# Performance work log

Measured on AMD Instinct MI355X. Metric: run time of the kernel, lower is better.

## Reference

```python
import jax, jax.numpy as jnp
import numpy as np

DIM = 1280
HEADS = 16
HD = DIM // HEADS  # 80
NSEG = 8
LSEG = 1024
SEQ = NSEG * LSEG  # 8192


def _rotate_half(x):
    x1, x2 = jnp.split(x, 2, axis=-1)
    return jnp.concatenate([-x2, x1], axis=-1)


def setup_inputs() -> dict:
    key = jax.random.key(0)
    ks = jax.random.split(key, 6)
    hidden_states = jax.random.normal(ks[0], (SEQ, DIM), dtype=jnp.float32)
    # rotary embedding table: per-position angles over head_dim
    inv_freq = 1.0 / (10000.0 ** (np.arange(0, HD, 2, dtype=np.float32) / HD))
    pos = np.arange(SEQ, dtype=np.float32)
    freqs = np.outer(pos, inv_freq)                    # [SEQ, HD/2]
    emb = np.concatenate([freqs, freqs], axis=-1)      # [SEQ, HD]
    cos = jnp.asarray(np.cos(emb), dtype=jnp.float32)
    sin = jnp.asarray(np.sin(emb), dtype=jnp.float32)
    w_scale = 1.0 / np.sqrt(DIM)
    qkv_w = jax.random.normal(ks[1], (DIM, 3 * DIM), dtype=jnp.float32) * w_scale
    qkv_b = jax.random.normal(ks[2], (3 * DIM,), dtype=jnp.float32) * 0.02
    proj_w = jax.random.normal(ks[3], (DIM, DIM), dtype=jnp.float32) * w_scale
    proj_b = jax.random.normal(ks[4], (DIM,), dtype=jnp.float32) * 0.02
    cu_seqlens = jnp.arange(NSEG + 1, dtype=jnp.int32) * LSEG
    return {
        "hidden_states": hidden_states,
        "cos": cos,
        "sin": sin,
        "qkv_w": qkv_w,
        "qkv_b": qkv_b,
        "proj_w": proj_w,
        "proj_b": proj_b,
        "cu_seqlens": cu_seqlens,
    }


def reference(hidden_states, cos, sin, qkv_w, qkv_b, proj_w, proj_b, cu_seqlens):
    S, D = hidden_states.shape
    n_seg = cu_seqlens.shape[0] - 1          # static
    L = S // n_seg                            # equal-length packed segments
    # fused QKV projection: [S, 3D] -> q, k, v each [S, H, hd]
    qkv = hidden_states @ qkv_w + qkv_b
    q, k, v = (t.reshape(S, HEADS, HD) for t in jnp.split(qkv, 3, axis=-1))
    # RoPE (computed in fp32, as in apply_rotary_pos_emb_vision)
    c = cos.astype(jnp.float32)[:, None, :]   # [S, 1, hd]
    s = sin.astype(jnp.float32)[:, None, :]
    qf = q.astype(jnp.float32)
    kf = k.astype(jnp.float32)
    q = (qf * c + _rotate_half(qf) * s).astype(q.dtype)
    k = (kf * c + _rotate_half(kf) * s).astype(k.dtype)
    # block-diagonal varlen attention == independent attention per segment
    qs = q.reshape(n_seg, L, HEADS, HD)
    ks = k.reshape(n_seg, L, HEADS, HD)
    vs = v.reshape(n_seg, L, HEADS, HD)
    scale = HD ** -0.5
    scores = jnp.einsum("nqhd,nkhd->nhqk", qs, ks) * scale
    probs = jax.nn.softmax(scores.astype(jnp.float32), axis=-1).astype(qs.dtype)
    out = jnp.einsum("nhqk,nkhd->nqhd", probs, vs)     # [n, L, H, hd]
    out = out.reshape(S, D)
    return out @ proj_w + proj_b
```

## Files before the change

### kernel.cpp

```cpp
#include <hip/hip_runtime.h>

#define SEQ   8192
#define DIM   1280
#define HEADS 16
#define HD    80
#define LSEG  1024
#define QKVD  3840

typedef unsigned short USHORT;
typedef __attribute__((ext_vector_type(8))) short bf16x8;
typedef __attribute__((ext_vector_type(4))) float f32x4;
typedef __attribute__((ext_vector_type(4))) USHORT u16x4;
typedef __attribute__((ext_vector_type(4))) int i32x4;

#define CSF  0.16129832f

__device__ __forceinline__ USHORT f2bf(float x) {
  unsigned u = __float_as_uint(x);
  u += 0x7fffu + ((u >> 16) & 1u);
  return (USHORT)(u >> 16);
}
__device__ __forceinline__ float bf2f(USHORT b) {
  return __uint_as_float(((unsigned)b) << 16);
}
__device__ __forceinline__ void gload16(const void* g, void* l) {
  __builtin_amdgcn_global_load_lds(
      (const __attribute__((address_space(1))) void*)g,
      (__attribute__((address_space(3))) void*)l, 16, 0, 0);
}
__device__ __forceinline__ unsigned cvtpk(float a, float b) {
  unsigned d;
  asm("v_cvt_pk_bf16_f32 %0, %1, %2" : "=v"(d) : "v"(a), "v"(b));
  return d;
}
#define SB() __builtin_amdgcn_sched_barrier(0)

__global__ __launch_bounds__(256) void prep1(
    const float* __restrict__ hs, USHORT* __restrict__ hsB,
    const float* __restrict__ qkv_w, USHORT* __restrict__ qkvwT,
    const float* __restrict__ proj_w, USHORT* __restrict__ pwT) {
  __shared__ float tb[32][33];
  const int bx = blockIdx.x;
  const int tid = threadIdx.x;
  if (bx < 10240) {
    const int i = bx * 256 + tid;
    const float4 v = reinterpret_cast<const float4*>(hs)[i];
    USHORT* o = hsB + (size_t)i * 4;
    o[0] = f2bf(v.x); o[1] = f2bf(v.y); o[2] = f2bf(v.z); o[3] = f2bf(v.w);
    return;
  }
  const float* W; USHORT* T; int K, N, n0, k0;
  if (bx < 15040) {
    const int b = bx - 10240;
    W = qkv_w; T = qkvwT; K = DIM; N = QKVD;
    n0 = (b % 120) * 32; k0 = (b / 120) * 32;
  } else {
    const int b = bx - 15040;
    W = proj_w; T = pwT; K = DIM; N = DIM;
    n0 = (b % 40) * 32; k0 = (b / 40) * 32;
  }
  const int c = tid & 31, r0 = tid >> 5;
  for (int r = r0; r < 32; r += 8) tb[r][c] = W[(size_t)(k0 + r) * N + n0 + c];
  __syncthreads();
  for (int r = r0; r < 32; r += 8)
    T[(size_t)(n0 + r) * K + k0 + c] = f2bf(tb[c][r]);
}

__global__ __launch_bounds__(256) void prep2(
    USHORT* __restrict__ qkv, const float* __restrict__ cosb,
    const float* __restrict__ sinb, uint4* __restrict__ zb) {
  const int bx = blockIdx.x;
  const int tid = threadIdx.x;
  if (bx < 10240) {
    int idx = bx * 256 + tid;
    const int d4 = (idx % 10) * 4;
    int t = idx / 10;
    const int h = t % HEADS;
    t /= HEADS;
    const int qk = t & 1;
    const int s = t >> 1;
    USHORT* base = qkv + (size_t)s * QKVD + qk * DIM + h * HD;
    const u16x4 x1 = *(const u16x4*)&base[d4];
    const u16x4 x2 = *(const u16x4*)&base[d4 + 40];
    const f32x4 c1 = *(const f32x4*)&cosb[s * HD + d4];
    const f32x4 s1 = *(const f32x4*)&sinb[s * HD + d4];
    const f32x4 c2 = *(const f32x4*)&cosb[s * HD + d4 + 40];
    const f32x4 s2 = *(const f32x4*)&sinb[s * HD + d4 + 40];
    u16x4 o1, o2;
#pragma unroll
    for (int j = 0; j < 4; ++j) {
      const float a = bf2f(x1[j]), b = bf2f(x2[j]);
      o1[j] = f2bf(a * c1[j] - b * s1[j]);
      o2[j] = f2bf(b * c2[j] + a * s2[j]);
    }
    *(u16x4*)&base[d4] = o1;
    *(u16x4*)&base[d4 + 40] = o2;
    return;
  }
  if (tid < 64) zb[tid] = uint4{0u, 0u, 0u, 0u};
}

__global__ __launch_bounds__(512, 1) void mfma_gemm256(
    const USHORT* __restrict__ Ah, const USHORT* __restrict__ Bh,
    const float* __restrict__ bias, USHORT* __restrict__ Cout,
    USHORT* __restrict__ VtGo, int M, int N, int K, int lda) {
  extern __shared__ USHORT sm[];

  const int tid = threadIdx.x;
  const int l = tid & 63;
  const int w = tid >> 6;
  const int fr = l & 15;
  const int g = l >> 4;
  const int nrow = M >> 8;
  const int nwg = nrow * (N >> 7);
  const int orig = blockIdx.x;
  const int wg = (orig & 7) * (nwg >> 3) + (orig >> 3);
  const int row0 = (wg % nrow) << 8;
  const int col0 = (wg / nrow) << 7;
  const int wr = (w >> 1) << 6;
  const int wc = (w & 1) << 6;

  const f32x4 fz = {0.f, 0.f, 0.f, 0.f};
  f32x4 acc[4][4];
#pragma unroll
  for (int m = 0; m < 4; ++m)
#pragma unroll
    for (int n = 0; n < 4; ++n) acc[m][n] = fz;

  const int NT = K >> 6;

  const USHORT* asrc[4];
  const USHORT* bsrc[2];
#pragma unroll
  for (int i = 0; i < 4; ++i) {
    const int u = i * 512 + tid;
    const int row = u >> 3;
    const int c = (u & 7) ^ (row & 7);
    asrc[i] = Ah + (size_t)(row0 + row) * lda + c * 8;
  }
#pragma unroll
  for (int i = 0; i < 2; ++i) {
    const int u = i * 512 + tid;
    const int row = u >> 3;
    const int c = (u & 7) ^ (row & 7);
    bsrc[i] = Bh + (size_t)(col0 + row) * K + c * 8;
  }
  auto stage = [&](int b) {
#pragma unroll
    for (int i = 0; i < 4; ++i)
      gload16(asrc[i], sm + b * 16384 + (i * 512 + (w << 6)) * 8);
#pragma unroll
    for (int i = 0; i < 2; ++i)
      gload16(bsrc[i], sm + 49152 + b * 8192 + (i * 512 + (w << 6)) * 8);
  };
  auto advance = [&]() {
#pragma unroll
    for (int i = 0; i < 4; ++i) asrc[i] += 64;
#pragma unroll
    for (int i = 0; i < 2; ++i) bsrc[i] += 64;
  };

  const int fb = fr & 7;
  int aOff[2], bOff[2];
#pragma unroll
  for (int ks = 0; ks < 2; ++ks) {
    const int sl = (((ks << 2) + g) ^ fb) << 3;
    aOff[ks] = (wr + fr) * 64 + sl;
    bOff[ks] = 49152 + (wc + fr) * 64 + sl;
  }

  stage(0); advance();
  stage(1); advance();

  int cur = 0, sb = 2;
  for (int t = 0; t < NT; ++t) {
    asm volatile("s_waitcnt vmcnt(6)" ::: "memory");
    SB();
    __builtin_amdgcn_s_barrier();
    SB();
    const int ca = cur * 16384, cbb = cur * 8192;
    bf16x8 ah[2][4], bh[2][4];
#pragma unroll
    for (int ks = 0; ks < 2; ++ks)
#pragma unroll
      for (int m = 0; m < 4; ++m) {
        ah[ks][m] = *(const bf16x8*)(sm + ca + aOff[ks] + m * 1024);
        bh[ks][m] = *(const bf16x8*)(sm + cbb + bOff[ks] + m * 1024);
      }
    stage(sb);
    if (t < NT - 3) advance();
    SB();
    asm volatile("s_waitcnt lgkmcnt(0)" ::: "memory");
    SB();
    __builtin_amdgcn_s_setprio(1);
#pragma unroll
    for (int ks = 0; ks < 2; ++ks)
#pragma unroll
      for (int m = 0; m < 4; ++m)
#pragma unroll
        for (int n = 0; n < 4; ++n)
          acc[m][n] = __builtin_amdgcn_mfma_f32_16x16x32_bf16(
              ah[ks][m], bh[ks][n], acc[m][n], 0, 0, 0);
    __builtin_amdgcn_s_setprio(0);
    cur = (cur == 2) ? 0 : cur + 1;
    sb = (sb == 2) ? 0 : sb + 1;
  }

  asm volatile("s_waitcnt vmcnt(0)" ::: "memory");

  float bv[4];
#pragma unroll
  for (int n = 0; n < 4; ++n) bv[n] = bias[col0 + wc + n * 16 + fr];
#pragma unroll
  for (int m = 0; m < 4; ++m)
#pragma unroll
    for (int n = 0; n < 4; ++n) {
      const int colb = col0 + wc + n * 16;
      const int row = row0 + wr + m * 16 + g * 4;
      if (colb >= 2 * DIM) {
        u16x4 o;
#pragma unroll
        for (int r = 0; r < 4; ++r) o[r] = f2bf(acc[m][n][r] + bv[n]);
        const int rl = row & 63;
        const int sc = (rl & 0x23) | ((rl & 0x10) >> 2) | ((rl & 0x0C) << 1);
        *(u16x4*)&VtGo[(size_t)(colb + fr - 2 * DIM) * SEQ + (row & ~63) + sc] = o;
      } else {
#pragma unroll
        for (int r = 0; r < 4; ++r)
          Cout[(size_t)(row + r) * N + colb + fr] = f2bf(acc[m][n][r] + bv[n]);
      }
    }
}

__global__ __launch_bounds__(256) void mfma_gemm(
    const USHORT* __restrict__ Ah, const USHORT* __restrict__ Bh,
    const float* __restrict__ bias, float* __restrict__ Cout,
    int M, int N, int K, int lda) {
  __shared__ __align__(16) USHORT AhL[2][8192];
  __shared__ __align__(16) USHORT BhL[2][8192];

  const int tid = threadIdx.x;
  const int l = tid & 63;
  const int w = tid >> 6;
  const int nrow = M >> 7;
  const int nwg = nrow * (N >> 7);
  const int orig = blockIdx.x;
  const int wg = (orig & 7) * (nwg >> 3) + (orig >> 3);
  const int row0 = (wg % nrow) << 7;
  const int col0 = (wg / nrow) << 7;
  const int wr = (w >> 1) << 6;
  const int wc = (w & 1) << 6;

  const f32x4 fz = {0.f, 0.f, 0.f, 0.f};
  f32x4 acc[4][4];
#pragma unroll
  for (int m = 0; m < 4; ++m)
#pragma unroll
    for (int n = 0; n < 4; ++n) acc[m][n] = fz;

  const int fr = l & 15;
  const int g = l >> 4;
  const int NT = K >> 6;

  const USHORT* asrc[4];
  const USHORT* bsrc[4];
#pragma unroll
  for (int i = 0; i < 4; ++i) {
    const int u = (w * 4 + i) * 64 + l;
    const int row = u >> 3;
    const int c = (u & 7) ^ (row & 7);
    asrc[i] = Ah + (size_t)(row0 + row) * lda + c * 8;
    bsrc[i] = Bh + (size_t)(col0 + row) * K + c * 8;
  }
  auto stage = [&](int b) {
#pragma unroll
    for (int i = 0; i < 4; ++i) {
      gload16(asrc[i], &AhL[b][(w * 4 + i) * 512]);
      gload16(bsrc[i], &BhL[b][(w * 4 + i) * 512]);
    }
  };
  auto advance = [&]() {
#pragma unroll
    for (int i = 0; i < 4; ++i) { asrc[i] += 64; bsrc[i] += 64; }
  };

  const int fb = fr & 7;
  int aOff[2], bOff[2];
#pragma unroll
  for (int ks = 0; ks < 2; ++ks) {
    const int sl = (((ks << 2) + g) ^ fb) << 3;
    aOff[ks] = (wr + fr) * 64 + sl;
    bOff[ks] = (wc + fr) * 64 + sl;
  }
  const USHORT* AB = &AhL[0][0];
  const USHORT* BB = &BhL[0][0];

  stage(0); advance();
  stage(1); advance();

  for (int t = 0; t < NT; ++t) {
    const int cur = t & 1;
    asm volatile("s_waitcnt vmcnt(8)" ::: "memory");
    SB();
    __builtin_amdgcn_s_barrier();
    SB();
    const int cb = cur << 13;
    bf16x8 ah[2][4], bh[2][4];
#pragma unroll
    for (int m = 0; m < 4; ++m) {
      ah[0][m] = *(const bf16x8*)(AB + cb + aOff[0] + m * 1024);
      bh[0][m] = *(const bf16x8*)(BB + cb + bOff[0] + m * 1024);
    }
    SB();
#pragma unroll
    for (int m = 0; m < 4; ++m) {
      ah[1][m] = *(const bf16x8*)(AB + cb + aOff[1] + m * 1024);
      bh[1][m] = *(const bf16x8*)(BB + cb + bOff[1] + m * 1024);
    }
    SB();
    asm volatile("s_waitcnt lgkmcnt(8)" ::: "memory");
    SB();
    __builtin_amdgcn_s_setprio(1);
#pragma unroll
    for (int m = 0; m < 4; ++m)
#pragma unroll
      for (int n = 0; n < 4; ++n)
        acc[m][n] = __builtin_amdgcn_mfma_f32_16x16x32_bf16(
            ah[0][m], bh[0][n], acc[m][n], 0, 0, 0);
    __builtin_amdgcn_s_setprio(0);
    SB();
    asm volatile("s_waitcnt lgkmcnt(0)" ::: "memory");
    SB();
    __builtin_amdgcn_s_barrier();
    SB();
    stage(cur);
    if (t < NT - 3) advance();
    SB();
    __builtin_amdgcn_s_setprio(1);
#pragma unroll
    for (int m = 0; m < 4; ++m)
#pragma unroll
      for (int n = 0; n < 4; ++n)
        acc[m][n] = __builtin_amdgcn_mfma_f32_16x16x32_bf16(
            ah[1][m], bh[1][n], acc[m][n], 0, 0, 0);
    __builtin_amdgcn_s_setprio(0);
  }

  asm volatile("s_waitcnt vmcnt(0)" ::: "memory");

  float bv[4];
#pragma unroll
  for (int n = 0; n < 4; ++n) bv[n] = bias[col0 + wc + n * 16 + fr];
#pragma unroll
  for (int m = 0; m < 4; ++m)
#pragma unroll
    for (int n = 0; n < 4; ++n)
#pragma unroll
      for (int r = 0; r < 4; ++r) {
        const float v = acc[m][n][r] + bv[n];
        const int row = row0 + wr + m * 16 + (l >> 4) * 4 + r;
        const int col = col0 + wc + n * 16 + fr;
        Cout[(size_t)row * N + col] = v;
      }
}

__global__ __launch_bounds__(256, 3) void attn_mfma9(
    const USHORT* __restrict__ qkv, const USHORT* __restrict__ VtG,
    const USHORT* __restrict__ zbuf, USHORT* __restrict__ aoB) {
  const int h = blockIdx.y;
  const int bx = blockIdx.x;
  const int qb = (bx & 7) * 8 + (bx >> 3);
  const int s0 = qb * 128;
  const int k0g = (s0 / LSEG) * LSEG;
  const int tid = threadIdx.x;
  const int w = tid >> 6, l = tid & 63;
  const int g = l >> 4, fr = l & 15;
  const int q0 = s0 + w * 32;

  __shared__ __align__(16) USHORT Kl[2][64 * 128];
  __shared__ __align__(16) USHORT Vl[2][80 * 64];

  bf16x8 qb_frag[2][3];
#pragma unroll
  for (int nt2 = 0; nt2 < 2; ++nt2)
#pragma unroll
    for (int ks = 0; ks < 3; ++ks)
      qb_frag[nt2][ks] = *(const bf16x8*)
          &qkv[(size_t)(q0 + nt2 * 16 + fr) * QKVD + h * HD + ks * 32 + g * 8];

  const f32x4 fz = {0.f, 0.f, 0.f, 0.f};
  f32x4 oacc[2][5];
#pragma unroll
  for (int m = 0; m < 2; ++m)
#pragma unroll
    for (int n = 0; n < 5; ++n) oacc[m][n] = fz;
  float l_run[2] = {0.f, 0.f};

  const int nV = (w < 2) ? 3 : 2;
  const int vbase = (w < 2) ? w * 3 : 6 + (w - 2) * 2;
  const USHORT* ksrc[4];
  int kstep[4];
#pragma unroll
  for (int i = 0; i < 4; ++i) {
    const int t = (w * 4 + i) * 64 + l;
    const int row = t >> 4, c = (t & 15) ^ (row & 7);
    if (c < 10) {
      ksrc[i] = qkv + (size_t)(k0g + row) * QKVD + DIM + h * HD + c * 8;
      kstep[i] = 64 * QKVD;
    } else {
      ksrc[i] = zbuf;
      kstep[i] = 0;
    }
  }
  const USHORT* vsrc[3] = {zbuf, zbuf, zbuf};
#pragma unroll
  for (int i = 0; i < 3; ++i)
    if (i < nV) {
      const int u = (vbase + i) * 64 + l;
      const int row = u >> 3, c = (u & 7) ^ (row & 7);
      vsrc[i] = VtG + (size_t)(h * HD + row) * SEQ + k0g + c * 8;
    }

  auto stageKV = [&](int kb, int b) {
#pragma unroll
    for (int i = 0; i < 4; ++i)
      gload16(ksrc[i] + (size_t)kb * kstep[i], &Kl[b][(w * 4 + i) * 512]);
#pragma unroll
    for (int i = 0; i < 3; ++i)
      if (i < nV)
        gload16(vsrc[i] + kb * 64, &Vl[b][(vbase + i) * 512]);
  };

  const int fb = fr & 7;
  int kOff[3], vOff[2];
#pragma unroll
  for (int ks = 0; ks < 3; ++ks)
    kOff[ks] = fr * 128 + ((((ks << 2) + g) ^ fb) << 3);
#pragma unroll
  for (int ks = 0; ks < 2; ++ks)
    vOff[ks] = fr * 64 + ((((ks << 2) + g) ^ fb) << 3);
  const USHORT* KB = &Kl[0][0];
  const USHORT* VB = &Vl[0][0];

  stageKV(0, 0);
  stageKV(1, 1);

  for (int kb = 0; kb < 16; ++kb) {
    const int cur = kb & 1;
    if (w < 2) {
      asm volatile("s_waitcnt vmcnt(7)" ::: "memory");
    } else {
      asm volatile("s_waitcnt vmcnt(6)" ::: "memory");
    }
    SB();
    __builtin_amdgcn_s_barrier();
    SB();
    const int kcb = cur << 13;
    const int vcb = cur * 5120;

    f32x4 sc[4][2];
#pragma unroll
    for (int m = 0; m < 4; ++m)
#pragma unroll
      for (int nt2 = 0; nt2 < 2; ++nt2) sc[m][nt2] = fz;
    __builtin_amdgcn_s_setprio(1);
#pragma unroll
    for (int ks = 0; ks < 3; ++ks)
#pragma unroll
      for (int m = 0; m < 4; ++m) {
        const bf16x8 kbf = *(const bf16x8*)(KB + kcb + kOff[ks] + m * 2048);
#pragma unroll
        for (int nt2 = 0; nt2 < 2; ++nt2)
          sc[m][nt2] = __builtin_amdgcn_mfma_f32_16x16x32_bf16(
              kbf, qb_frag[nt2][ks], sc[m][nt2], 0, 0, 0);
      }
    __builtin_amdgcn_s_setprio(0);

    unsigned pkr[2][4][2];
#pragma unroll
    for (int nt2 = 0; nt2 < 2; ++nt2) {
      float ps = 0.f;
#pragma unroll
      for (int m = 0; m < 4; ++m) {
        float p[4];
#pragma unroll
        for (int j = 0; j < 4; ++j) {
          p[j] = exp2f(sc[m][nt2][j] * CSF);
          ps += p[j];
        }
        pkr[nt2][m][0] = cvtpk(p[0], p[1]);
        pkr[nt2][m][1] = cvtpk(p[2], p[3]);
      }
      ps += __shfl_xor(ps, 16);
      ps += __shfl_xor(ps, 32);
      l_run[nt2] += ps;
    }

#pragma unroll
    for (int ks = 0; ks < 2; ++ks) {
      union { bf16x8 v8; i32x4 i4; } pa[2];
#pragma unroll
      for (int mt2 = 0; mt2 < 2; ++mt2) {
        pa[mt2].i4[0] = (int)pkr[mt2][2 * ks][0];
        pa[mt2].i4[1] = (int)pkr[mt2][2 * ks][1];
        pa[mt2].i4[2] = (int)pkr[mt2][2 * ks + 1][0];
        pa[mt2].i4[3] = (int)pkr[mt2][2 * ks + 1][1];
      }
      __builtin_amdgcn_s_setprio(1);
#pragma unroll
      for (int nt = 0; nt < 5; ++nt) {
        const bf16x8 vb = *(const bf16x8*)(VB + vcb + vOff[ks] + nt * 1024);
#pragma unroll
        for (int mt2 = 0; mt2 < 2; ++mt2)
          oacc[mt2][nt] = __builtin_amdgcn_mfma_f32_16x16x32_bf16(
              pa[mt2].v8, vb, oacc[mt2][nt], 0, 0, 0);
      }
      __builtin_amdgcn_s_setprio(0);
    }

    __builtin_amdgcn_s_barrier();
    SB();
    const int kn = (kb + 2 < 16) ? kb + 2 : kb;
    stageKV(kn, cur);
    SB();
  }

  asm volatile("s_waitcnt vmcnt(0)" ::: "memory");

  float linv[2][4];
#pragma unroll
  for (int mt2 = 0; mt2 < 2; ++mt2)
#pragma unroll
    for (int j = 0; j < 4; ++j)
      linv[mt2][j] = 1.f / __shfl(l_run[mt2], 20 * g + j);
#pragma unroll
  for (int mt2 = 0; mt2 < 2; ++mt2)
#pragma unroll
    for (int nt = 0; nt < 5; ++nt)
#pragma unroll
      for (int j = 0; j < 4; ++j) {
        const int row = s0 + w * 32 + mt2 * 16 + g * 4 + j;
        const int col = h * HD + nt * 16 + fr;
        aoB[(size_t)row * QKVD + col] = f2bf(oacc[mt2][nt][j] * linv[mt2][j]);
      }
}

extern "C" void kernel_launch(void* const* d_in, const int* in_sizes, int n_in,
                              void* d_out, int out_size, void* d_ws,
                              size_t ws_size, hipStream_t stream) {
  const float* hs = (const float*)d_in[0];
  const float* cosb = (const float*)d_in[1];
  const float* sinb = (const float*)d_in[2];
  const float* qkv_w = (const float*)d_in[3];
  const float* qkv_b = (const float*)d_in[4];
  const float* proj_w = (const float*)d_in[5];
  const float* proj_b = (const float*)d_in[6];
  char* ws = (char*)d_ws;

  USHORT* qkvB  = (USHORT*)(ws);
  USHORT* hsB   = (USHORT*)(ws + 62914560u);
  USHORT* qkvwT = (USHORT*)(ws + 83886080u);
  USHORT* pwT   = (USHORT*)(ws + 93716480u);
  USHORT* VtG   = (USHORT*)d_out;
  USHORT* zbuf  = qkvwT;
  USHORT* aoB   = qkvB + 2 * DIM;

  hipFuncSetAttribute((const void*)mfma_gemm256,
                      hipFuncAttributeMaxDynamicSharedMemorySize, 147456);

  prep1<<<16640, 256, 0, stream>>>(hs, hsB, qkv_w, qkvwT, proj_w, pwT);
  mfma_gemm256<<<(SEQ / 256) * (QKVD / 128), 512, 147456, stream>>>(
      hsB, qkvwT, qkv_b, qkvB, VtG, SEQ, QKVD, DIM, DIM);
  prep2<<<10241, 256, 0, stream>>>(qkvB, cosb, sinb, (uint4*)zbuf);
  attn_mfma9<<<dim3(SEQ / 128, HEADS), 256, 0, stream>>>(qkvB, VtG, zbuf, aoB);
  mfma_gemm<<<(SEQ / 128) * (DIM / 128), 256, 0, stream>>>(
      aoB, pwT, proj_b, (float*)d_out, SEQ, DIM, DIM, QKVD);
}
```

Before: 304.6 us.

## Retile QKV GEMM to 256x256 output tiles with K-step 32

The QKV projection GEMM moves from 256x128 tiles with a 64-wide K step to 256x256 tiles with a 32-wide K step. Each wave now computes a 128x64 sub-tile with 8x4 accumulators, and A/B staging shares one 16 KB buffer per stage with a new XOR swizzle. Larger tiles raise arithmetic intensity and cut redundant global loads of A, and shared memory per block drops. The cost is twice as many barriers per K element, higher register pressure, and fewer workgroups (480) to spread across the CUs.

```diff
diff --git a/kernel.cpp b/kernel.cpp
--- a/kernel.cpp
+++ b/kernel.cpp
@@ -112,81 +112,67 @@
   const int fr = l & 15;
   const int g = l >> 4;
   const int nrow = M >> 8;
-  const int nwg = nrow * (N >> 7);
+  const int nwg = nrow * (N >> 8);
   const int orig = blockIdx.x;
   const int wg = (orig & 7) * (nwg >> 3) + (orig >> 3);
   const int row0 = (wg % nrow) << 8;
-  const int col0 = (wg / nrow) << 7;
-  const int wr = (w >> 1) << 6;
-  const int wc = (w & 1) << 6;
+  const int col0 = (wg / nrow) << 8;
+  const int wr = (w >> 2) << 7;
+  const int wc = (w & 3) << 6;
 
   const f32x4 fz = {0.f, 0.f, 0.f, 0.f};
-  f32x4 acc[4][4];
-#pragma unroll
-  for (int m = 0; m < 4; ++m)
+  f32x4 acc[8][4];
+#pragma unroll
+  for (int m = 0; m < 8; ++m)
 #pragma unroll
     for (int n = 0; n < 4; ++n) acc[m][n] = fz;
 
-  const int NT = K >> 6;
-
-  const USHORT* asrc[4];
+  const int NT = K >> 5;
+
+  const USHORT* asrc[2];
   const USHORT* bsrc[2];
-#pragma unroll
-  for (int i = 0; i < 4; ++i) {
-    const int u = i * 512 + tid;
-    const int row = u >> 3;
-    const int c = (u & 7) ^ (row & 7);
-    asrc[i] = Ah + (size_t)(row0 + row) * lda + c * 8;
-  }
 #pragma unroll
   for (int i = 0; i < 2; ++i) {
     const int u = i * 512 + tid;
-    const int row = u >> 3;
-    const int c = (u & 7) ^ (row & 7);
+    const int row = u >> 2;
+    const int c = (u & 3) ^ ((row >> 1) & 3);
+    asrc[i] = Ah + (size_t)(row0 + row) * lda + c * 8;
     bsrc[i] = Bh + (size_t)(col0 + row) * K + c * 8;
   }
   auto stage = [&](int b) {
 #pragma unroll
-    for (int i = 0; i < 4; ++i)
-      gload16(asrc[i], sm + b * 16384 + (i * 512 + (w << 6)) * 8);
-#pragma unroll
-    for (int i = 0; i < 2; ++i)
-      gload16(bsrc[i], sm + 49152 + b * 8192 + (i * 512 + (w << 6)) * 8);
+    for (int i = 0; i < 2; ++i) {
+      USHORT* dst = sm + b * 16384 + (i * 512 + (w << 6)) * 8;
+      gload16(asrc[i], dst);
+      gload16(bsrc[i], dst + 8192);
+    }
   };
   auto advance = [&]() {
 #pragma unroll
-    for (int i = 0; i < 4; ++i) asrc[i] += 64;
-#pragma unroll
-    for (int i = 0; i < 2; ++i) bsrc[i] += 64;
+    for (int i = 0; i < 2; ++i) { asrc[i] += 32; bsrc[i] += 32; }
   };
 
-  const int fb = fr & 7;
-  int aOff[2], bOff[2];
-#pragma unroll
-  for (int ks = 0; ks < 2; ++ks) {
-    const int sl = (((ks << 2) + g) ^ fb) << 3;
-    aOff[ks] = (wr + fr) * 64 + sl;
-    bOff[ks] = 49152 + (wc + fr) * 64 + sl;
-  }
+  const int sl = (g ^ ((fr >> 1) & 3)) << 3;
+  const int aBase = (wr + fr) * 32 + sl;
+  const int bBase = 8192 + (wc + fr) * 32 + sl;
 
   stage(0); advance();
   stage(1); advance();
 
   int cur = 0, sb = 2;
   for (int t = 0; t < NT; ++t) {
-    asm volatile("s_waitcnt vmcnt(6)" ::: "memory");
+    asm volatile("s_waitcnt vmcnt(4)" ::: "memory");
     SB();
     __builtin_amdgcn_s_barrier();
     SB();
-    const int ca = cur * 16384, cbb = cur * 8192;
-    bf16x8 ah[2][4], bh[2][4];
-#pragma unroll
-    for (int ks = 0; ks < 2; ++ks)
-#pragma unroll
-      for (int m = 0; m < 4; ++m) {
-        ah[ks][m] = *(const bf16x8*)(sm + ca + aOff[ks] + m * 1024);
-        bh[ks][m] = *(const bf16x8*)(sm + cbb + bOff[ks] + m * 1024);
-      }
+    const int cb = cur * 16384;
+    bf16x8 ah[8], bh[4];
+#pragma unroll
+    for (int m = 0; m < 8; ++m)
+      ah[m] = *(const bf16x8*)(sm + cb + aBase + m * 512);
+#pragma unroll
+    for (int n = 0; n < 4; ++n)
+      bh[n] = *(const bf16x8*)(sm + cb + bBase + n * 512);
     stage(sb);
     if (t < NT - 3) advance();
     SB();
@@ -194,13 +180,11 @@
     SB();
     __builtin_amdgcn_s_setprio(1);
 #pragma unroll
-    for (int ks = 0; ks < 2; ++ks)
-#pragma unroll
-      for (int m = 0; m < 4; ++m)
-#pragma unroll
-        for (int n = 0; n < 4; ++n)
-          acc[m][n] = __builtin_amdgcn_mfma_f32_16x16x32_bf16(
-              ah[ks][m], bh[ks][n], acc[m][n], 0, 0, 0);
+    for (int m = 0; m < 8; ++m)
+#pragma unroll
+      for (int n = 0; n < 4; ++n)
+        acc[m][n] = __builtin_amdgcn_mfma_f32_16x16x32_bf16(
+            ah[m], bh[n], acc[m][n], 0, 0, 0);
     __builtin_amdgcn_s_setprio(0);
     cur = (cur == 2) ? 0 : cur + 1;
     sb = (sb == 2) ? 0 : sb + 1;
@@ -212,7 +196,7 @@
 #pragma unroll
   for (int n = 0; n < 4; ++n) bv[n] = bias[col0 + wc + n * 16 + fr];
 #pragma unroll
-  for (int m = 0; m < 4; ++m)
+  for (int m = 0; m < 8; ++m)
 #pragma unroll
     for (int n = 0; n < 4; ++n) {
       const int colb = col0 + wc + n * 16;
@@ -566,10 +550,10 @@
   USHORT* aoB   = qkvB + 2 * DIM;
 
   hipFuncSetAttribute((const void*)mfma_gemm256,
-                      hipFuncAttributeMaxDynamicSharedMemorySize, 147456);
+                      hipFuncAttributeMaxDynamicSharedMemorySize, 98304);
 
   prep1<<<16640, 256, 0, stream>>>(hs, hsB, qkv_w, qkvwT, proj_w, pwT);
-  mfma_gemm256<<<(SEQ / 256) * (QKVD / 128), 512, 147456, stream>>>(
+  mfma_gemm256<<<(SEQ / 256) * (QKVD / 256), 512, 98304, stream>>>(
       hsB, qkvwT, qkv_b, qkvB, VtG, SEQ, QKVD, DIM, DIM);
   prep2<<<10241, 256, 0, stream>>>(qkvB, cosb, sinb, (uint4*)zbuf);
   attn_mfma9<<<dim3(SEQ / 128, HEADS), 256, 0, stream>>>(qkvB, VtG, zbuf, aoB);
```

Measured after the change: 257.0 us. -15.6%, faster.
